# Performance work log

Hardware: AMD Instinct MI355X
Metric: run time of the kernel (lower is better)

Reference implementation:

```python
import jax, jax.numpy as jnp
import numpy as np

B, S, D_IN, D = 2, 4096, 1024, 64  # batch, seq_len, input_dim, head dim d


def setup_inputs() -> dict:
    key = jax.random.key(0)
    k1, k2, k3, k4 = jax.random.split(key, 4)
    X = jax.random.normal(k1, (B, S, D_IN), dtype=jnp.float32)
    W_q = jax.random.normal(k2, (D_IN, 2 * D), dtype=jnp.float32) / np.sqrt(D_IN)
    W_k = jax.random.normal(k3, (D_IN, 2 * D), dtype=jnp.float32) / np.sqrt(D_IN)
    W_v = jax.random.normal(k4, (D_IN, 2 * D), dtype=jnp.float32) / np.sqrt(D_IN)
    lam = jnp.float32(0.8)
    return {"X": X, "W_q": W_q, "W_k": W_k, "W_v": W_v, "lam": lam}


def reference(X, W_q, W_k, W_v, lam):
    d = W_q.shape[-1] // 2
    Q = X @ W_q  # [B, S, 2d]
    K = X @ W_k  # [B, S, 2d]
    V = X @ W_v  # [B, S, 2d]
    Q1, Q2 = Q[..., :d], Q[..., d:]
    K1, K2 = K[..., :d], K[..., d:]
    s = 1.0 / jnp.sqrt(jnp.float32(d))
    A1 = jnp.einsum("bqd,bkd->bqk", Q1, K1) * s  # [B, S, S]
    A2 = jnp.einsum("bqd,bkd->bqk", Q2, K2) * s  # [B, S, S]
    P = jax.nn.softmax(A1, axis=-1) - lam * jax.nn.softmax(A2, axis=-1)
    return jnp.einsum("bqk,bkv->bqv", P, V)  # [B, S, 2d]
```

## Files before the change

### kernel.cpp

```cpp
#include <hip/hip_runtime.h>
#include <hip/hip_bf16.h>

typedef float f32x4 __attribute__((ext_vector_type(4)));
typedef float f32x16 __attribute__((ext_vector_type(16)));
typedef short bf16x8 __attribute__((ext_vector_type(8)));

#define MFMA16(A,B,C) __builtin_amdgcn_mfma_f32_16x16x32_bf16(A,B,C,0,0,0)
#define MFMA32(A,B,C) __builtin_amdgcn_mfma_f32_32x32x16_bf16(A,B,C,0,0,0)

__device__ __forceinline__ unsigned short f2bf(float f) {
    union { float f; unsigned u; } x; x.f = f;
    return (unsigned short)((x.u + 0x7FFFu + ((x.u >> 16) & 1u)) >> 16);
}

__device__ __forceinline__ unsigned fbits(float f) {
    union { float f; unsigned u; } x; x.f = f; return x.u;
}

__device__ __forceinline__ f32x16 zero16() {
    f32x16 z;
#pragma unroll
    for (int i = 0; i < 16; ++i) z[i] = 0.f;
    return z;
}

typedef const __attribute__((address_space(1))) unsigned int* as1_t;
typedef __attribute__((address_space(3))) unsigned int* as3_t;
__device__ __forceinline__ void gl_lds16(const unsigned short* g, unsigned short* l) {
    __builtin_amdgcn_global_load_lds((as1_t)g, (as3_t)l, 16, 0, 0);
}

__global__ void prep_wt(const float* __restrict__ Wq, const float* __restrict__ Wk,
                        const float* __restrict__ Wv, unsigned short* __restrict__ WT) {
    int w = blockIdx.x % 3;
    int kt = blockIdx.x / 3;
    const float* src = (w == 0) ? Wq : (w == 1) ? Wk : Wv;
    int k0 = kt * 32;
#pragma unroll
    for (int j = 0; j < 16; ++j) {
        int idx = threadIdx.x + j * 256;
        int r = idx >> 7, c = idx & 127;
        float v = src[(size_t)(k0 + r) * 128 + c];
        WT[(size_t)(w * 128 + c) * 1024 + k0 + r] = f2bf(v);
    }
}

__global__ __launch_bounds__(256) void prep_x(const float* __restrict__ X,
                                              unsigned short* __restrict__ Xb) {
    int i = blockIdx.x * 256 + threadIdx.x;
#pragma unroll
    for (int r = 0; r < 8; ++r) {
        int idx = i + r * 262144;
        float4 x = ((const float4*)X)[idx];
        ushort4 p;
        p.x = f2bf(x.x); p.y = f2bf(x.y); p.z = f2bf(x.z); p.w = f2bf(x.w);
        ((ushort4*)Xb)[idx] = p;
    }
}

__global__ __launch_bounds__(256) void proj(const unsigned short* __restrict__ Xb,
        const unsigned short* __restrict__ WT, unsigned short* __restrict__ Qc,
        unsigned short* __restrict__ Kc, unsigned short* __restrict__ VT) {
    int tid = threadIdx.x;
    int w = tid >> 6, lane = tid & 63;
    int lr = lane & 15, lg = lane >> 4;
    int wr = w >> 1, wc = w & 1;
    int m0 = blockIdx.x * 64;
    int n0 = blockIdx.y * 96;

    __shared__ __align__(16) unsigned short Ab[2][64 * 64];
    __shared__ __align__(16) unsigned short Bb[2][96 * 64];

    f32x4 acc[2][3];
#pragma unroll
    for (int i = 0; i < 2; ++i)
#pragma unroll
        for (int j = 0; j < 3; ++j) acc[i][j] = f32x4{0.f,0.f,0.f,0.f};

    int srow = lane >> 3;
    int sunit = lane & 7;
    const unsigned short* aSrc = Xb + (size_t)(m0 + srow) * 1024 + sunit * 8;
    const unsigned short* bSrc = WT + (size_t)(n0 + srow) * 1024 + sunit * 8;

    auto STAGE = [&](int bsel, int st) {
        int kk = st * 64;
#pragma unroll
        for (int i = 0; i < 2; ++i) {
            int blk = w * 2 + i;
            gl_lds16(aSrc + (size_t)blk * 8 * 1024 + kk, &Ab[bsel][blk * 512]);
        }
#pragma unroll
        for (int i = 0; i < 3; ++i) {
            int blk = w * 3 + i;
            gl_lds16(bSrc + (size_t)blk * 8 * 1024 + kk, &Bb[bsel][blk * 512]);
        }
    };

    STAGE(0, 0);
    __syncthreads();

    for (int st = 0; st < 16; ++st) {
        int cur = st & 1;
        if (st + 1 < 16) STAGE(cur ^ 1, st + 1);

        const unsigned short* ab = &Ab[cur][0];
        const unsigned short* bb = &Bb[cur][0];
#pragma unroll
        for (int ksub = 0; ksub < 2; ++ksub) {
            int ko = ksub * 32 + lg * 8;
            bf16x8 af[2], bf[3];
#pragma unroll
            for (int mt = 0; mt < 2; ++mt)
                af[mt] = *(const bf16x8*)(ab + (wr * 32 + mt * 16 + lr) * 64 + ko);
#pragma unroll
            for (int nt = 0; nt < 3; ++nt)
                bf[nt] = *(const bf16x8*)(bb + (wc * 48 + nt * 16 + lr) * 64 + ko);
#pragma unroll
            for (int mt = 0; mt < 2; ++mt)
#pragma unroll
                for (int nt = 0; nt < 3; ++nt)
                    acc[mt][nt] = MFMA16(af[mt], bf[nt], acc[mt][nt]);
        }
        __syncthreads();
    }

    int b = m0 >> 12;
    int sbase = (m0 & 4095) + wr * 32;
#pragma unroll
    for (int nt = 0; nt < 3; ++nt) {
        int gcol = n0 + wc * 48 + nt * 16 + lr;
        int tensor = gcol >> 7;
#pragma unroll
        for (int mt = 0; mt < 2; ++mt) {
            int sloc = sbase + mt * 16 + 4 * lg;
            if (tensor == 2) {
                int vcol = gcol & 127;
                int slocV = (sloc & ~15) | (((lg & 1) << 3) | ((lg >> 1) << 2));
                ushort4 pk;
                pk.x = f2bf(acc[mt][nt][0]); pk.y = f2bf(acc[mt][nt][1]);
                pk.z = f2bf(acc[mt][nt][2]); pk.w = f2bf(acc[mt][nt][3]);
                *(ushort4*)(VT + (size_t)(b * 128 + vcol) * 4096 + slocV) = pk;
            } else {
                int within = gcol & 127;
                int comp = within >> 6;
                int col64 = within & 63;
                float sc = (tensor == 0) ? 0.1803368801f : 1.0f;
                unsigned short* dst = (tensor == 0) ? Qc : Kc;
                size_t rowb = (size_t)(comp * 2 + b) * 4096 + sloc;
#pragma unroll
                for (int r = 0; r < 4; ++r)
                    dst[(rowb + r) * 64 + col64] = f2bf(acc[mt][nt][r] * sc);
            }
        }
    }
}

__global__ __launch_bounds__(256, 2) void attn(const unsigned short* __restrict__ Qc,
        const unsigned short* __restrict__ Kc, const unsigned short* __restrict__ VT,
        float* __restrict__ Opart, float* __restrict__ Lpart) {
    int tid = threadIdx.x;
    int wave = tid >> 6, lane = tid & 63;
    int l31 = lane & 31, hi = lane >> 5;
    int x7 = l31 & 7;
    int b = blockIdx.y;
    int comp = blockIdx.z >> 2, split = blockIdx.z & 3;
    int q0 = blockIdx.x * 128 + wave * 32;
    int kstart = split * 1024;

    __shared__ __align__(16) unsigned short kbuf[2][64 * 64];
    __shared__ __align__(16) unsigned short vbuf[2][128 * 64];

    const unsigned short* Qp = Qc + ((size_t)(comp * 2 + b) * 4096 + q0 + l31) * 64 + hi * 8;
    bf16x8 qB0 = *(const bf16x8*)(Qp);
    bf16x8 qB1 = *(const bf16x8*)(Qp + 16);
    bf16x8 qB2 = *(const bf16x8*)(Qp + 32);
    bf16x8 qB3 = *(const bf16x8*)(Qp + 48);

    f32x16 o[4];
#pragma unroll
    for (int i = 0; i < 4; ++i) o[i] = zero16();
    f32x16 ol = zero16();
    bf16x8 ones;
#pragma unroll
    for (int i = 0; i < 8; ++i) ones[i] = (short)0x3F80;

    int swz = (lane & 7) ^ (lane >> 3);
    const unsigned short* kSrc = Kc + ((size_t)(comp * 2 + b) * 4096 + kstart
                                       + wave * 8 + (lane >> 3)) * 64 + swz * 8;
    const unsigned short* vSrc = VT + ((size_t)b * 128 + (tid >> 3)) * 4096
                                    + kstart + swz * 8;

    auto STAGE = [&](int bsel, int it) {
        const unsigned short* ks = kSrc + (size_t)it * 4096;
        gl_lds16(ks,        &kbuf[bsel][wave * 512]);
        gl_lds16(ks + 2048, &kbuf[bsel][2048 + wave * 512]);
        const unsigned short* vs = vSrc + it * 64;
#pragma unroll
        for (int ri = 0; ri < 4; ++ri)
            gl_lds16(vs + (size_t)ri * 32 * 4096, &vbuf[bsel][ri * 2048 + wave * 512]);
    };

    STAGE(0, 0);
    __syncthreads();

    for (int it = 0; it < 16; ++it) {
        int cur = it & 1;
        if (it + 1 < 16) STAGE(cur ^ 1, it + 1);

        const unsigned short* kb = &kbuf[cur][0];
        const unsigned short* vb = &vbuf[cur][0];

        f32x16 st0 = zero16(), st1 = zero16();
        __builtin_amdgcn_s_setprio(1);
#pragma unroll
        for (int j = 0; j < 4; ++j) {
            int ku = ((j * 2 + hi) ^ x7) * 8;
            bf16x8 kA0 = *(const bf16x8*)(kb + l31 * 64 + ku);
            bf16x8 kA1 = *(const bf16x8*)(kb + (32 + l31) * 64 + ku);
            bf16x8 qj = (j == 0) ? qB0 : (j == 1) ? qB1 : (j == 2) ? qB2 : qB3;
            st0 = MFMA32(kA0, qj, st0);
            st1 = MFMA32(kA1, qj, st1);
        }
        __builtin_amdgcn_s_setprio(0);

        union W4 { unsigned u[4]; bf16x8 v; };
        W4 wA0, wB0, wA1, wB1;
#pragma unroll
        for (int i2 = 0; i2 < 4; ++i2) {
            float a0 = __builtin_amdgcn_exp2f(st0[2 * i2]);
            float a1 = __builtin_amdgcn_exp2f(st0[2 * i2 + 1]);
            float a2 = __builtin_amdgcn_exp2f(st0[8 + 2 * i2]);
            float a3 = __builtin_amdgcn_exp2f(st0[9 + 2 * i2]);
            float b0 = __builtin_amdgcn_exp2f(st1[2 * i2]);
            float b1 = __builtin_amdgcn_exp2f(st1[2 * i2 + 1]);
            float b2 = __builtin_amdgcn_exp2f(st1[8 + 2 * i2]);
            float b3 = __builtin_amdgcn_exp2f(st1[9 + 2 * i2]);
            wA0.u[i2] = __builtin_amdgcn_perm(fbits(a1), fbits(a0), 0x07060302);
            wB0.u[i2] = __builtin_amdgcn_perm(fbits(a3), fbits(a2), 0x07060302);
            wA1.u[i2] = __builtin_amdgcn_perm(fbits(b1), fbits(b0), 0x07060302);
            wB1.u[i2] = __builtin_amdgcn_perm(fbits(b3), fbits(b2), 0x07060302);
        }

        __builtin_amdgcn_s_setprio(1);
        ol = MFMA32(wA0.v, ones, ol);
        ol = MFMA32(wB0.v, ones, ol);
        ol = MFMA32(wA1.v, ones, ol);
        ol = MFMA32(wB1.v, ones, ol);
#pragma unroll
        for (int vt = 0; vt < 4; ++vt) {
            const unsigned short* vrow = vb + (vt * 32 + l31) * 64;
            o[vt] = MFMA32(wA0.v, *(const bf16x8*)(vrow + ((0 + hi) ^ x7) * 8), o[vt]);
            o[vt] = MFMA32(wB0.v, *(const bf16x8*)(vrow + ((2 + hi) ^ x7) * 8), o[vt]);
            o[vt] = MFMA32(wA1.v, *(const bf16x8*)(vrow + ((4 + hi) ^ x7) * 8), o[vt]);
            o[vt] = MFMA32(wB1.v, *(const bf16x8*)(vrow + ((6 + hi) ^ x7) * 8), o[vt]);
        }
        __builtin_amdgcn_s_setprio(0);
        __syncthreads();
    }

    int base = (b * 2 + comp) * 4 + split;
    float* op = Opart + (size_t)base * 4096 * 128;
#pragma unroll
    for (int vt = 0; vt < 4; ++vt)
#pragma unroll
        for (int r = 0; r < 16; ++r) {
            int qr = (r & 3) + 8 * (r >> 2) + 4 * hi;
            op[(size_t)(q0 + qr) * 128 + vt * 32 + l31] = o[vt][r];
        }
    if (l31 == 0) {
        float* lp = Lpart + (size_t)base * 4096 + q0;
#pragma unroll
        for (int r = 0; r < 16; ++r)
            lp[(r & 3) + 8 * (r >> 2) + 4 * hi] = ol[r];
    }
}

__global__ __launch_bounds__(256) void combine(const float* __restrict__ Opart,
        const float* __restrict__ Lpart, const float* __restrict__ lamp,
        float* __restrict__ out) {
    float lam = lamp[0];
    int i = blockIdx.x * 256 + threadIdx.x;
    int row = i >> 5;
    int c4  = i & 31;
    int b = row >> 12, q = row & 4095;

    float l1 = 0.f, l2 = 0.f;
#pragma unroll
    for (int s = 0; s < 4; ++s) {
        l1 += Lpart[((b * 2 + 0) * 4 + s) * 4096 + q];
        l2 += Lpart[((b * 2 + 1) * 4 + s) * 4096 + q];
    }
    float rl1 = 1.0f / l1, rl2 = 1.0f / l2;

    size_t chunk = (size_t)4096 * 32;
    size_t fi = (size_t)q * 32 + c4;
    const float4* Obase = (const float4*)Opart + (size_t)b * 8 * chunk;
    float4 a = Obase[fi];
    float4 c = Obase[4 * chunk + fi];
#pragma unroll
    for (int s = 1; s < 4; ++s) {
        float4 t1 = Obase[s * chunk + fi];
        float4 t2 = Obase[(4 + s) * chunk + fi];
        a.x += t1.x; a.y += t1.y; a.z += t1.z; a.w += t1.w;
        c.x += t2.x; c.y += t2.y; c.z += t2.z; c.w += t2.w;
    }
    float4 r;
    r.x = a.x * rl1 - lam * c.x * rl2;
    r.y = a.y * rl1 - lam * c.y * rl2;
    r.z = a.z * rl1 - lam * c.z * rl2;
    r.w = a.w * rl1 - lam * c.w * rl2;
    ((float4*)out)[i] = r;
}

extern "C" void kernel_launch(void* const* d_in, const int* in_sizes, int n_in,
                              void* d_out, int out_size, void* d_ws, size_t ws_size,
                              hipStream_t stream) {
    const float* X   = (const float*)d_in[0];
    const float* Wq  = (const float*)d_in[1];
    const float* Wk  = (const float*)d_in[2];
    const float* Wv  = (const float*)d_in[3];
    const float* lam = (const float*)d_in[4];
    float* out = (float*)d_out;

    char* ws = (char*)d_ws;
    unsigned short* Qc = (unsigned short*)(ws);
    unsigned short* Kc = (unsigned short*)(ws + 2097152);
    unsigned short* VT = (unsigned short*)(ws + 4194304);
    unsigned short* WT = (unsigned short*)(ws + 6291456);
    unsigned short* Xb = (unsigned short*)(ws + 7077888);
    float* Opart = (float*)(ws + 6291456);
    float* Lpart = (float*)(ws + 39845888);

    prep_wt<<<dim3(96), dim3(256), 0, stream>>>(Wq, Wk, Wv, WT);
    prep_x<<<dim3(1024), dim3(256), 0, stream>>>(X, Xb);
    proj<<<dim3(128, 4), dim3(256), 0, stream>>>(Xb, WT, Qc, Kc, VT);
    attn<<<dim3(32, 2, 8), dim3(256), 0, stream>>>(Qc, Kc, VT, Opart, Lpart);
    combine<<<dim3(1024), dim3(256), 0, stream>>>(Opart, Lpart, lam, out);
}
```

Before: 81.09 us.

## Split waves across query and value-column groups with 64-row query tiles

Reassigns waves so each processes 64 query rows and half of the 128 value columns, instead of 32 rows and all columns. This halves per-wave V fragment LDS reads and reuses K fragments across two query groups. In exchange, the QK^T scores and exponentials are computed redundantly by both value-column waves, and register use grows. Only one wave per query group accumulates the row sums.

Measured after the change: 88.32 us. 8.9% more time.

```diff
diff --git a/kernel.cpp b/kernel.cpp
--- a/kernel.cpp
+++ b/kernel.cpp
@@ -164,31 +164,37 @@
     int x7 = l31 & 7;
     int b = blockIdx.y;
     int comp = blockIdx.z >> 2, split = blockIdx.z & 3;
-    int q0 = blockIdx.x * 128 + wave * 32;
+    int qg = wave & 1, vg = wave >> 1;
+    int q0 = blockIdx.x * 128 + qg * 64;
     int kstart = split * 1024;
 
     __shared__ __align__(16) unsigned short kbuf[2][64 * 64];
     __shared__ __align__(16) unsigned short vbuf[2][128 * 64];
 
-    const unsigned short* Qp = Qc + ((size_t)(comp * 2 + b) * 4096 + q0 + l31) * 64 + hi * 8;
-    bf16x8 qB0 = *(const bf16x8*)(Qp);
-    bf16x8 qB1 = *(const bf16x8*)(Qp + 16);
-    bf16x8 qB2 = *(const bf16x8*)(Qp + 32);
-    bf16x8 qB3 = *(const bf16x8*)(Qp + 48);
-
-    f32x16 o[4];
-#pragma unroll
-    for (int i = 0; i < 4; ++i) o[i] = zero16();
-    f32x16 ol = zero16();
+    const unsigned short* Qbase = Qc + ((size_t)(comp * 2 + b) * 4096 + q0 + l31) * 64 + hi * 8;
+    bf16x8 qB[2][4];
+#pragma unroll
+    for (int g = 0; g < 2; ++g)
+#pragma unroll
+        for (int j = 0; j < 4; ++j)
+            qB[g][j] = *(const bf16x8*)(Qbase + g * 32 * 64 + j * 16);
+
+    f32x16 o[2][2];
+#pragma unroll
+    for (int g = 0; g < 2; ++g)
+#pragma unroll
+        for (int vt = 0; vt < 2; ++vt) o[g][vt] = zero16();
+    f32x16 ol[2];
+    ol[0] = zero16(); ol[1] = zero16();
     bf16x8 ones;
 #pragma unroll
     for (int i = 0; i < 8; ++i) ones[i] = (short)0x3F80;
 
-    int swz = (lane & 7) ^ (lane >> 3);
     const unsigned short* kSrc = Kc + ((size_t)(comp * 2 + b) * 4096 + kstart
-                                       + wave * 8 + (lane >> 3)) * 64 + swz * 8;
+                                       + wave * 8 + (lane >> 3)) * 64
+                                    + ((lane & 7) ^ (lane >> 3)) * 8;
     const unsigned short* vSrc = VT + ((size_t)b * 128 + (tid >> 3)) * 4096
-                                    + kstart + swz * 8;
+                                    + kstart + ((lane & 7) ^ (lane >> 3)) * 8;
 
     auto STAGE = [&](int bsel, int it) {
         const unsigned short* ks = kSrc + (size_t)it * 4096;
@@ -210,49 +216,70 @@
         const unsigned short* kb = &kbuf[cur][0];
         const unsigned short* vb = &vbuf[cur][0];
 
-        f32x16 st0 = zero16(), st1 = zero16();
+        f32x16 st00 = zero16(), st01 = zero16(), st10 = zero16(), st11 = zero16();
         __builtin_amdgcn_s_setprio(1);
 #pragma unroll
         for (int j = 0; j < 4; ++j) {
             int ku = ((j * 2 + hi) ^ x7) * 8;
             bf16x8 kA0 = *(const bf16x8*)(kb + l31 * 64 + ku);
             bf16x8 kA1 = *(const bf16x8*)(kb + (32 + l31) * 64 + ku);
-            bf16x8 qj = (j == 0) ? qB0 : (j == 1) ? qB1 : (j == 2) ? qB2 : qB3;
-            st0 = MFMA32(kA0, qj, st0);
-            st1 = MFMA32(kA1, qj, st1);
+            st00 = MFMA32(kA0, qB[0][j], st00);
+            st01 = MFMA32(kA1, qB[0][j], st01);
+            st10 = MFMA32(kA0, qB[1][j], st10);
+            st11 = MFMA32(kA1, qB[1][j], st11);
         }
         __builtin_amdgcn_s_setprio(0);
 
         union W4 { unsigned u[4]; bf16x8 v; };
-        W4 wA0, wB0, wA1, wB1;
-#pragma unroll
-        for (int i2 = 0; i2 < 4; ++i2) {
-            float a0 = __builtin_amdgcn_exp2f(st0[2 * i2]);
-            float a1 = __builtin_amdgcn_exp2f(st0[2 * i2 + 1]);
-            float a2 = __builtin_amdgcn_exp2f(st0[8 + 2 * i2]);
-            float a3 = __builtin_amdgcn_exp2f(st0[9 + 2 * i2]);
-            float b0 = __builtin_amdgcn_exp2f(st1[2 * i2]);
-            float b1 = __builtin_amdgcn_exp2f(st1[2 * i2 + 1]);
-            float b2 = __builtin_amdgcn_exp2f(st1[8 + 2 * i2]);
-            float b3 = __builtin_amdgcn_exp2f(st1[9 + 2 * i2]);
-            wA0.u[i2] = __builtin_amdgcn_perm(fbits(a1), fbits(a0), 0x07060302);
-            wB0.u[i2] = __builtin_amdgcn_perm(fbits(a3), fbits(a2), 0x07060302);
-            wA1.u[i2] = __builtin_amdgcn_perm(fbits(b1), fbits(b0), 0x07060302);
-            wB1.u[i2] = __builtin_amdgcn_perm(fbits(b3), fbits(b2), 0x07060302);
+        W4 wP[2][4];
+#pragma unroll
+        for (int g = 0; g < 2; ++g) {
+            const f32x16& s0 = g ? st10 : st00;
+            const f32x16& s1 = g ? st11 : st01;
+#pragma unroll
+            for (int i2 = 0; i2 < 4; ++i2) {
+                float a0 = __builtin_amdgcn_exp2f(s0[2 * i2]);
+                float a1 = __builtin_amdgcn_exp2f(s0[2 * i2 + 1]);
+                float a2 = __builtin_amdgcn_exp2f(s0[8 + 2 * i2]);
+                float a3 = __builtin_amdgcn_exp2f(s0[9 + 2 * i2]);
+                float b0 = __builtin_amdgcn_exp2f(s1[2 * i2]);
+                float b1 = __builtin_amdgcn_exp2f(s1[2 * i2 + 1]);
+                float b2 = __builtin_amdgcn_exp2f(s1[8 + 2 * i2]);
+                float b3 = __builtin_amdgcn_exp2f(s1[9 + 2 * i2]);
+                wP[g][0].u[i2] = __builtin_amdgcn_perm(fbits(a1), fbits(a0), 0x07060302);
+                wP[g][1].u[i2] = __builtin_amdgcn_perm(fbits(a3), fbits(a2), 0x07060302);
+                wP[g][2].u[i2] = __builtin_amdgcn_perm(fbits(b1), fbits(b0), 0x07060302);
+                wP[g][3].u[i2] = __builtin_amdgcn_perm(fbits(b3), fbits(b2), 0x07060302);
+            }
+        }
+
+        if (vg == 0) {
+            __builtin_amdgcn_s_setprio(1);
+#pragma unroll
+            for (int g = 0; g < 2; ++g) {
+                ol[g] = MFMA32(wP[g][0].v, ones, ol[g]);
+                ol[g] = MFMA32(wP[g][1].v, ones, ol[g]);
+                ol[g] = MFMA32(wP[g][2].v, ones, ol[g]);
+                ol[g] = MFMA32(wP[g][3].v, ones, ol[g]);
+            }
+            __builtin_amdgcn_s_setprio(0);
         }
 
         __builtin_amdgcn_s_setprio(1);
-        ol = MFMA32(wA0.v, ones, ol);
-        ol = MFMA32(wB0.v, ones, ol);
-        ol = MFMA32(wA1.v, ones, ol);
-        ol = MFMA32(wB1.v, ones, ol);
-#pragma unroll
-        for (int vt = 0; vt < 4; ++vt) {
-            const unsigned short* vrow = vb + (vt * 32 + l31) * 64;
-            o[vt] = MFMA32(wA0.v, *(const bf16x8*)(vrow + ((0 + hi) ^ x7) * 8), o[vt]);
-            o[vt] = MFMA32(wB0.v, *(const bf16x8*)(vrow + ((2 + hi) ^ x7) * 8), o[vt]);
-            o[vt] = MFMA32(wA1.v, *(const bf16x8*)(vrow + ((4 + hi) ^ x7) * 8), o[vt]);
-            o[vt] = MFMA32(wB1.v, *(const bf16x8*)(vrow + ((6 + hi) ^ x7) * 8), o[vt]);
+#pragma unroll
+        for (int vt = 0; vt < 2; ++vt) {
+            const unsigned short* vrow = vb + (vg * 64 + vt * 32 + l31) * 64;
+            bf16x8 v0 = *(const bf16x8*)(vrow + ((0 + hi) ^ x7) * 8);
+            bf16x8 v1 = *(const bf16x8*)(vrow + ((2 + hi) ^ x7) * 8);
+            bf16x8 v2 = *(const bf16x8*)(vrow + ((4 + hi) ^ x7) * 8);
+            bf16x8 v3 = *(const bf16x8*)(vrow + ((6 + hi) ^ x7) * 8);
+#pragma unroll
+            for (int g = 0; g < 2; ++g) {
+                o[g][vt] = MFMA32(wP[g][0].v, v0, o[g][vt]);
+                o[g][vt] = MFMA32(wP[g][1].v, v1, o[g][vt]);
+                o[g][vt] = MFMA32(wP[g][2].v, v2, o[g][vt]);
+                o[g][vt] = MFMA32(wP[g][3].v, v3, o[g][vt]);
+            }
         }
         __builtin_amdgcn_s_setprio(0);
         __syncthreads();
@@ -261,17 +288,21 @@
     int base = (b * 2 + comp) * 4 + split;
     float* op = Opart + (size_t)base * 4096 * 128;
 #pragma unroll
-    for (int vt = 0; vt < 4; ++vt)
-#pragma unroll
-        for (int r = 0; r < 16; ++r) {
-            int qr = (r & 3) + 8 * (r >> 2) + 4 * hi;
-            op[(size_t)(q0 + qr) * 128 + vt * 32 + l31] = o[vt][r];
-        }
-    if (l31 == 0) {
+    for (int g = 0; g < 2; ++g)
+#pragma unroll
+        for (int vt = 0; vt < 2; ++vt)
+#pragma unroll
+            for (int r = 0; r < 16; ++r) {
+                int qr = (r & 3) + 8 * (r >> 2) + 4 * hi;
+                op[(size_t)(q0 + g * 32 + qr) * 128 + vg * 64 + vt * 32 + l31] = o[g][vt][r];
+            }
+    if (vg == 0 && l31 == 0) {
         float* lp = Lpart + (size_t)base * 4096 + q0;
 #pragma unroll
-        for (int r = 0; r < 16; ++r)
-            lp[(r & 3) + 8 * (r >> 2) + 4 * hi] = ol[r];
+        for (int g = 0; g < 2; ++g)
+#pragma unroll
+            for (int r = 0; r < 16; ++r)
+                lp[g * 32 + (r & 3) + 8 * (r >> 2) + 4 * hi] = ol[g][r];
     }
 }
 
```

## Triple-buffer proj/attn LDS pipelines and store partial outputs in bf16

Applied to the files above, without the earlier changes.

The proj and attn kernels move from double to triple buffering. The per-iteration __syncthreads becomes a single s_barrier preceded by a partial vmcnt wait, so two stages of global-to-LDS loads stay in flight. Separately, the attention partial outputs are written as bf16 instead of fp32, which halves the write and read traffic between attn and combine. The costs are more LDS per block, which may limit occupancy of attn (launch bounds ask for 2 blocks per CU), and lower precision in the partial sums.

New measurement: 75.33 us. 1.08x faster.

```diff
diff --git a/kernel.cpp b/kernel.cpp
--- a/kernel.cpp
+++ b/kernel.cpp
@@ -11,6 +11,10 @@
 __device__ __forceinline__ unsigned short f2bf(float f) {
     union { float f; unsigned u; } x; x.f = f;
     return (unsigned short)((x.u + 0x7FFFu + ((x.u >> 16) & 1u)) >> 16);
+}
+
+__device__ __forceinline__ float bf2f(unsigned short u) {
+    union { unsigned u; float f; } x; x.u = ((unsigned)u) << 16; return x.f;
 }
 
 __device__ __forceinline__ unsigned fbits(float f) {
@@ -68,8 +72,8 @@
     int m0 = blockIdx.x * 64;
     int n0 = blockIdx.y * 96;
 
-    __shared__ __align__(16) unsigned short Ab[2][64 * 64];
-    __shared__ __align__(16) unsigned short Bb[2][96 * 64];
+    __shared__ __align__(16) unsigned short Ab[3][64 * 64];
+    __shared__ __align__(16) unsigned short Bb[3][96 * 64];
 
     f32x4 acc[2][3];
 #pragma unroll
@@ -82,29 +86,35 @@
     const unsigned short* aSrc = Xb + (size_t)(m0 + srow) * 1024 + sunit * 8;
     const unsigned short* bSrc = WT + (size_t)(n0 + srow) * 1024 + sunit * 8;
 
-    auto STAGE = [&](int bsel, int st) {
+    auto STAGE = [&](unsigned short* ad, unsigned short* bd, int st) {
         int kk = st * 64;
 #pragma unroll
         for (int i = 0; i < 2; ++i) {
             int blk = w * 2 + i;
-            gl_lds16(aSrc + (size_t)blk * 8 * 1024 + kk, &Ab[bsel][blk * 512]);
+            gl_lds16(aSrc + (size_t)blk * 8 * 1024 + kk, ad + blk * 512);
         }
 #pragma unroll
         for (int i = 0; i < 3; ++i) {
             int blk = w * 3 + i;
-            gl_lds16(bSrc + (size_t)blk * 8 * 1024 + kk, &Bb[bsel][blk * 512]);
+            gl_lds16(bSrc + (size_t)blk * 8 * 1024 + kk, bd + blk * 512);
         }
     };
 
-    STAGE(0, 0);
-    __syncthreads();
+    unsigned short *a0 = Ab[0], *a1 = Ab[1], *a2 = Ab[2];
+    unsigned short *b0 = Bb[0], *b1 = Bb[1], *b2 = Bb[2];
+    STAGE(a0, b0, 0);
+    STAGE(a1, b1, 1);
 
     for (int st = 0; st < 16; ++st) {
-        int cur = st & 1;
-        if (st + 1 < 16) STAGE(cur ^ 1, st + 1);
-
-        const unsigned short* ab = &Ab[cur][0];
-        const unsigned short* bb = &Bb[cur][0];
+        if (st < 15) asm volatile("s_waitcnt vmcnt(5)" ::: "memory");
+        else         asm volatile("s_waitcnt vmcnt(0)" ::: "memory");
+        __builtin_amdgcn_sched_barrier(0);
+        __builtin_amdgcn_s_barrier();
+        __builtin_amdgcn_sched_barrier(0);
+        if (st + 2 < 16) STAGE(a2, b2, st + 2);
+
+        const unsigned short* ab = a0;
+        const unsigned short* bb = b0;
 #pragma unroll
         for (int ksub = 0; ksub < 2; ++ksub) {
             int ko = ksub * 32 + lg * 8;
@@ -121,7 +131,9 @@
                 for (int nt = 0; nt < 3; ++nt)
                     acc[mt][nt] = MFMA16(af[mt], bf[nt], acc[mt][nt]);
         }
-        __syncthreads();
+        unsigned short* t;
+        t = a0; a0 = a1; a1 = a2; a2 = t;
+        t = b0; b0 = b1; b1 = b2; b2 = t;
     }
 
     int b = m0 >> 12;
@@ -157,7 +169,7 @@
 
 __global__ __launch_bounds__(256, 2) void attn(const unsigned short* __restrict__ Qc,
         const unsigned short* __restrict__ Kc, const unsigned short* __restrict__ VT,
-        float* __restrict__ Opart, float* __restrict__ Lpart) {
+        unsigned short* __restrict__ Opart, float* __restrict__ Lpart) {
     int tid = threadIdx.x;
     int wave = tid >> 6, lane = tid & 63;
     int l31 = lane & 31, hi = lane >> 5;
@@ -167,8 +179,8 @@
     int q0 = blockIdx.x * 128 + wave * 32;
     int kstart = split * 1024;
 
-    __shared__ __align__(16) unsigned short kbuf[2][64 * 64];
-    __shared__ __align__(16) unsigned short vbuf[2][128 * 64];
+    __shared__ __align__(16) unsigned short kb3[3][64 * 64];
+    __shared__ __align__(16) unsigned short vb3[3][128 * 64];
 
     const unsigned short* Qp = Qc + ((size_t)(comp * 2 + b) * 4096 + q0 + l31) * 64 + hi * 8;
     bf16x8 qB0 = *(const bf16x8*)(Qp);
@@ -184,31 +196,37 @@
 #pragma unroll
     for (int i = 0; i < 8; ++i) ones[i] = (short)0x3F80;
 
-    int swz = (lane & 7) ^ (lane >> 3);
     const unsigned short* kSrc = Kc + ((size_t)(comp * 2 + b) * 4096 + kstart
-                                       + wave * 8 + (lane >> 3)) * 64 + swz * 8;
+                                       + wave * 8 + (lane >> 3)) * 64
+                                    + ((lane & 7) ^ (lane >> 3)) * 8;
     const unsigned short* vSrc = VT + ((size_t)b * 128 + (tid >> 3)) * 4096
-                                    + kstart + swz * 8;
-
-    auto STAGE = [&](int bsel, int it) {
+                                    + kstart + ((lane & 7) ^ (lane >> 3)) * 8;
+
+    auto STAGE = [&](unsigned short* kd, unsigned short* vd, int it) {
         const unsigned short* ks = kSrc + (size_t)it * 4096;
-        gl_lds16(ks,        &kbuf[bsel][wave * 512]);
-        gl_lds16(ks + 2048, &kbuf[bsel][2048 + wave * 512]);
+        gl_lds16(ks,        kd + wave * 512);
+        gl_lds16(ks + 2048, kd + 2048 + wave * 512);
         const unsigned short* vs = vSrc + it * 64;
 #pragma unroll
         for (int ri = 0; ri < 4; ++ri)
-            gl_lds16(vs + (size_t)ri * 32 * 4096, &vbuf[bsel][ri * 2048 + wave * 512]);
+            gl_lds16(vs + (size_t)ri * 32 * 4096, vd + ri * 2048 + wave * 512);
     };
 
-    STAGE(0, 0);
-    __syncthreads();
+    unsigned short *k0 = kb3[0], *k1 = kb3[1], *k2 = kb3[2];
+    unsigned short *v0 = vb3[0], *v1 = vb3[1], *v2 = vb3[2];
+    STAGE(k0, v0, 0);
+    STAGE(k1, v1, 1);
 
     for (int it = 0; it < 16; ++it) {
-        int cur = it & 1;
-        if (it + 1 < 16) STAGE(cur ^ 1, it + 1);
-
-        const unsigned short* kb = &kbuf[cur][0];
-        const unsigned short* vb = &vbuf[cur][0];
+        if (it < 15) asm volatile("s_waitcnt vmcnt(6)" ::: "memory");
+        else         asm volatile("s_waitcnt vmcnt(0)" ::: "memory");
+        __builtin_amdgcn_sched_barrier(0);
+        __builtin_amdgcn_s_barrier();
+        __builtin_amdgcn_sched_barrier(0);
+        if (it + 2 < 16) STAGE(k2, v2, it + 2);
+
+        const unsigned short* kb = k0;
+        const unsigned short* vb = v0;
 
         f32x16 st0 = zero16(), st1 = zero16();
         __builtin_amdgcn_s_setprio(1);
@@ -255,17 +273,20 @@
             o[vt] = MFMA32(wB1.v, *(const bf16x8*)(vrow + ((6 + hi) ^ x7) * 8), o[vt]);
         }
         __builtin_amdgcn_s_setprio(0);
-        __syncthreads();
+
+        unsigned short* t;
+        t = k0; k0 = k1; k1 = k2; k2 = t;
+        t = v0; v0 = v1; v1 = v2; v2 = t;
     }
 
     int base = (b * 2 + comp) * 4 + split;
-    float* op = Opart + (size_t)base * 4096 * 128;
+    unsigned short* op = Opart + (size_t)base * 4096 * 128;
 #pragma unroll
     for (int vt = 0; vt < 4; ++vt)
 #pragma unroll
         for (int r = 0; r < 16; ++r) {
             int qr = (r & 3) + 8 * (r >> 2) + 4 * hi;
-            op[(size_t)(q0 + qr) * 128 + vt * 32 + l31] = o[vt][r];
+            op[(size_t)(q0 + qr) * 128 + vt * 32 + l31] = f2bf(o[vt][r]);
         }
     if (l31 == 0) {
         float* lp = Lpart + (size_t)base * 4096 + q0;
@@ -275,7 +296,7 @@
     }
 }
 
-__global__ __launch_bounds__(256) void combine(const float* __restrict__ Opart,
+__global__ __launch_bounds__(256) void combine(const unsigned short* __restrict__ Opart,
         const float* __restrict__ Lpart, const float* __restrict__ lamp,
         float* __restrict__ out) {
     float lam = lamp[0];
@@ -287,28 +308,26 @@
     float l1 = 0.f, l2 = 0.f;
 #pragma unroll
     for (int s = 0; s < 4; ++s) {
-        l1 += Lpart[((b * 2 + 0) * 4 + s) * 4096 + q];
-        l2 += Lpart[((b * 2 + 1) * 4 + s) * 4096 + q];
+        l1 += Lpart[((size_t)((b * 2 + 0) * 4 + s)) * 4096 + q];
+        l2 += Lpart[((size_t)((b * 2 + 1) * 4 + s)) * 4096 + q];
     }
     float rl1 = 1.0f / l1, rl2 = 1.0f / l2;
 
-    size_t chunk = (size_t)4096 * 32;
-    size_t fi = (size_t)q * 32 + c4;
-    const float4* Obase = (const float4*)Opart + (size_t)b * 8 * chunk;
-    float4 a = Obase[fi];
-    float4 c = Obase[4 * chunk + fi];
-#pragma unroll
-    for (int s = 1; s < 4; ++s) {
-        float4 t1 = Obase[s * chunk + fi];
-        float4 t2 = Obase[(4 + s) * chunk + fi];
-        a.x += t1.x; a.y += t1.y; a.z += t1.z; a.w += t1.w;
-        c.x += t2.x; c.y += t2.y; c.z += t2.z; c.w += t2.w;
+    size_t qoff = (size_t)q * 128 + c4 * 4;
+    float a0 = 0.f, a1 = 0.f, a2 = 0.f, a3 = 0.f;
+    float c0 = 0.f, c1 = 0.f, c2 = 0.f, c3 = 0.f;
+#pragma unroll
+    for (int s = 0; s < 4; ++s) {
+        ushort4 p1 = *(const ushort4*)(Opart + (size_t)((b * 2 + 0) * 4 + s) * 4096 * 128 + qoff);
+        ushort4 p2 = *(const ushort4*)(Opart + (size_t)((b * 2 + 1) * 4 + s) * 4096 * 128 + qoff);
+        a0 += bf2f(p1.x); a1 += bf2f(p1.y); a2 += bf2f(p1.z); a3 += bf2f(p1.w);
+        c0 += bf2f(p2.x); c1 += bf2f(p2.y); c2 += bf2f(p2.z); c3 += bf2f(p2.w);
     }
     float4 r;
-    r.x = a.x * rl1 - lam * c.x * rl2;
-    r.y = a.y * rl1 - lam * c.y * rl2;
-    r.z = a.z * rl1 - lam * c.z * rl2;
-    r.w = a.w * rl1 - lam * c.w * rl2;
+    r.x = a0 * rl1 - lam * c0 * rl2;
+    r.y = a1 * rl1 - lam * c1 * rl2;
+    r.z = a2 * rl1 - lam * c2 * rl2;
+    r.w = a3 * rl1 - lam * c3 * rl2;
     ((float4*)out)[i] = r;
 }
 
@@ -328,8 +347,8 @@
     unsigned short* VT = (unsigned short*)(ws + 4194304);
     unsigned short* WT = (unsigned short*)(ws + 6291456);
     unsigned short* Xb = (unsigned short*)(ws + 7077888);
-    float* Opart = (float*)(ws + 6291456);
-    float* Lpart = (float*)(ws + 39845888);
+    unsigned short* Opart = (unsigned short*)(ws + 6291456);
+    float* Lpart = (float*)(ws + 23068672);
 
     prep_wt<<<dim3(96), dim3(256), 0, stream>>>(Wq, Wk, Wv, WT);
     prep_x<<<dim3(1024), dim3(256), 0, stream>>>(X, Xb);
```
